# Kernel tuning notes

Hardware: AMD Instinct MI355X
Metric: run time of the kernel (lower is better)

## Reference

```python
import jax, jax.numpy as jnp
import numpy as np

N, E = 100000, 1600000
IN_F, HID, OUT_F, HEADS = 256, 128, 64, 1
C = HID // HEADS  # per-head channels (=128 for heads=1)
NEG_SLOPE = 0.2   # PyG GATConv default leaky_relu slope


def setup_inputs() -> dict:
    key = jax.random.key(0)
    ks = jax.random.split(key, 16)
    w = lambda k, shape, fan: (jax.random.normal(k, shape, jnp.float32) / np.float32(np.sqrt(fan)))
    return {
        "x": jax.random.normal(ks[0], (N, IN_F), jnp.float32),
        "edge_index": jax.random.randint(ks[1], (2, E), 0, N, dtype=jnp.int32),
        "W_in": w(ks[2], (IN_F, HID), IN_F),
        "b_in": jnp.zeros((HID,), jnp.float32),
        "W1": w(ks[3], (HID, HEADS * C), HID),
        "att_src1": w(ks[4], (HEADS, C), C),
        "att_dst1": w(ks[5], (HEADS, C), C),
        "bias1": jnp.zeros((C,), jnp.float32),
        "W2": w(ks[6], (HID, HEADS * C), HID),
        "att_src2": w(ks[7], (HEADS, C), C),
        "att_dst2": w(ks[8], (HEADS, C), C),
        "bias2": jnp.zeros((C,), jnp.float32),
        "W_out": w(ks[9], (HID, OUT_F), HID),
        "b_out": jnp.zeros((OUT_F,), jnp.float32),
    }


def gat_conv(h, src, dst, W, a_src, a_dst, bias):
    """PyG GATConv, concat=False: per-head attention, segment softmax over dst, mean over heads."""
    g = (h @ W).reshape(-1, HEADS, C)                      # [N,H,C]
    alpha_src = jnp.einsum("nhc,hc->nh", g, a_src)         # [N,H]
    alpha_dst = jnp.einsum("nhc,hc->nh", g, a_dst)         # [N,H]
    e = jax.nn.leaky_relu(alpha_src[src] + alpha_dst[dst], NEG_SLOPE)  # [E,H]
    m = jax.ops.segment_max(e, dst, num_segments=N)        # [N,H], -inf for empty segments
    m = jnp.where(jnp.isfinite(m), m, 0.0)
    p = jnp.exp(e - m[dst])
    s = jax.ops.segment_sum(p, dst, num_segments=N)        # [N,H]
    alpha = p / (s[dst] + 1e-16)                           # [E,H]
    msg = g[src] * alpha[..., None]                        # [E,H,C]  (dominant traffic)
    out = jax.ops.segment_sum(msg, dst, num_segments=N)    # [N,H,C]
    return out.mean(axis=1) + bias                         # concat=False -> head average


def reference(x, edge_index, W_in, b_in, W1, att_src1, att_dst1, bias1,
              W2, att_src2, att_dst2, bias2, W_out, b_out):
    src, dst = edge_index[0], edge_index[1]
    h = x @ W_in + b_in
    h = jax.nn.relu(gat_conv(h, src, dst, W1, att_src1, att_dst1, bias1))
    h = jax.nn.relu(gat_conv(h, src, dst, W2, att_src2, att_dst2, bias2))
    return h @ W_out + b_out
```

## Files before the change

### kernel.cpp

```cpp
#include <hip/hip_runtime.h>
#include <hip/hip_fp16.h>
#include <math.h>

#define NN 100000
#define EE 1600000
constexpr int IN_F = 256, HID = 128, OUT_F = 64;

#define NB 196
#define CAP 16384
#define CH 16384
#define NCHUNK 98

typedef __bf16 bf16x8 __attribute__((ext_vector_type(8)));
typedef float  f32x4  __attribute__((ext_vector_type(4)));

__device__ __forceinline__ f32x4 mfma16(bf16x8 a, bf16x8 b, f32x4 c){
  return __builtin_amdgcn_mfma_f32_16x16x32_bf16(a, b, c, 0, 0, 0);
}

__device__ __forceinline__ float wred_max(float v){
#pragma unroll
  for (int m=1; m<64; m<<=1) v = fmaxf(v, __shfl_xor(v, m, 64));
  return v;
}
__device__ __forceinline__ float wred_sum(float v){
#pragma unroll
  for (int m=1; m<64; m<<=1) v += __shfl_xor(v, m, 64);
  return v;
}

__global__ __launch_bounds__(256) void k_bin(const int* __restrict__ src,
    const int* __restrict__ dst, int* __restrict__ bucketCnt, int* __restrict__ recs)
{
  __shared__ int sd[CH];
  __shared__ int cnt[NB];
  __shared__ int base[NB];
  const int tid = threadIdx.x;
  const int e0 = blockIdx.x * CH;
  const int ne = min(CH, EE - e0);

  for (int i=tid; i<NB; i+=256) cnt[i] = 0;
  __syncthreads();
  for (int i=tid; i<ne; i+=256){
    int d = dst[e0+i];
    sd[i] = d;
    atomicAdd(&cnt[d>>9], 1);
  }
  __syncthreads();
  for (int i=tid; i<NB; i+=256) base[i] = atomicAdd(&bucketCnt[i], cnt[i]);
  __syncthreads();
  for (int i=tid; i<NB; i+=256) cnt[i] = 0;
  __syncthreads();
  for (int i=tid; i<ne; i+=256){
    int d = sd[i], b = d >> 9;
    int r = atomicAdd(&cnt[b], 1);
    int pos = base[b] + r;
    if (pos < CAP) recs[(size_t)b*CAP + pos] = src[e0+i] | ((d & 511) << 17);
  }
}

__global__ void k_bscan(const int* __restrict__ bucketCnt, int* __restrict__ bucketStart){
  __shared__ int sd[256];
  int t = threadIdx.x;
  int v = (t < NB) ? min(bucketCnt[t], CAP) : 0;
  sd[t] = v; __syncthreads();
#pragma unroll
  for (int off=1; off<256; off<<=1){
    int x = (t >= off) ? sd[t-off] : 0;
    __syncthreads();
    sd[t] += x;
    __syncthreads();
  }
  if (t < NB) bucketStart[t] = sd[t] - v;
}

__global__ __launch_bounds__(256) void k_csr(const int* __restrict__ recs,
    const int* __restrict__ bucketCnt, const int* __restrict__ bucketStart,
    int* __restrict__ rp, int* __restrict__ colsrc)
{
  __shared__ int hist[513];
  __shared__ int srcbuf[CAP];
  const int tid = threadIdx.x;
  const int b = blockIdx.x;
  const int cntb = min(bucketCnt[b], CAP);
  const int bstart = bucketStart[b];
  const int n0 = b << 9;
  const int nnode = min(512, NN - n0);
  const int* rb = recs + (size_t)b*CAP;

  for (int i=tid; i<513; i+=256) hist[i] = 0;
  __syncthreads();
  for (int i=tid; i<cntb; i+=256) atomicAdd(&hist[(rb[i] >> 17) + 1], 1);
  __syncthreads();
#pragma unroll
  for (int off=1; off<513; off<<=1){
    int vals[3];
    int q = 0;
    for (int i=tid; i<513; i+=256, q++) vals[q] = (i >= off) ? hist[i-off] : 0;
    __syncthreads();
    q = 0;
    for (int i=tid; i<513; i+=256, q++) hist[i] += vals[q];
    __syncthreads();
  }
  for (int l=tid; l<nnode; l+=256) rp[n0+l] = bstart + hist[l];
  if (b == 0 && tid == 0) rp[NN] = EE;
  __syncthreads();
  for (int i=tid; i<cntb; i+=256){
    int rec = rb[i];
    int r = atomicAdd(&hist[rec >> 17], 1);
    srcbuf[r] = rec & 0x1FFFF;
  }
  __syncthreads();
  for (int i=tid; i<cntb; i+=256) colsrc[bstart + i] = srcbuf[i];
}

__global__ void k_wsplit(const float* __restrict__ W, __bf16* __restrict__ hi, __bf16* __restrict__ lo,
                         int K, int N){
  int idx = blockIdx.x*256 + threadIdx.x;
  if (idx >= K*N) return;
  int k = idx / N, n = idx - k*N;
  float v = W[idx];
  __bf16 h = (__bf16)v;
  hi[(size_t)n*K + k] = h;
  lo[(size_t)n*K + k] = (__bf16)(v - (float)h);
}

template<int K, int BN, bool ATT, bool BIAS, typename OT>
__global__ __launch_bounds__(256) void k_gemm_mfma(
    const float* __restrict__ A, const __bf16* __restrict__ Bhi, const __bf16* __restrict__ Blo,
    const float* __restrict__ bias, OT* __restrict__ C,
    const float* __restrict__ attS, const float* __restrict__ attD,
    float* __restrict__ asrc, float* __restrict__ adst, int nrows)
{
  constexpr int NF = BN/16;
  __shared__ float  As[64][36];
  __shared__ __bf16 Bh[BN][56];
  __shared__ __bf16 Bl[BN][56];
  const int tid  = threadIdx.x;
  const int w    = tid >> 6, lane = tid & 63;
  const int lr   = lane & 15, lk = (lane >> 4) * 8;
  const int rowBase = blockIdx.x * 64;

  f32x4 acc[NF];
#pragma unroll
  for (int i=0;i<NF;i++) acc[i] = (f32x4)(0.f);

  const int ar = tid >> 2, aq = tid & 3;
  int agr = rowBase + ar; if (agr >= nrows) agr = nrows - 1;
  const float* aptr = A + (size_t)agr*K + aq*8;
  const int bn = tid >> 1, bhalf = tid & 1;
  const bool bact = (tid < BN*2);

  for (int kc=0; kc<K; kc+=32){
    float4 av0 = *(const float4*)(aptr + kc);
    float4 av1 = *(const float4*)(aptr + kc + 4);
    bf16x8 bh0, bh1, bl0, bl1;
    if (bact){
      const __bf16* ph = Bhi + (size_t)bn*K + kc + bhalf*16;
      const __bf16* pl = Blo + (size_t)bn*K + kc + bhalf*16;
      bh0 = *(const bf16x8*)(ph);
      bh1 = *(const bf16x8*)(ph + 8);
      bl0 = *(const bf16x8*)(pl);
      bl1 = *(const bf16x8*)(pl + 8);
    }
    __syncthreads();
    *(float4*)&As[ar][aq*8]     = av0;
    *(float4*)&As[ar][aq*8 + 4] = av1;
    if (bact){
      *(bf16x8*)&Bh[bn][bhalf*16]     = bh0;
      *(bf16x8*)&Bh[bn][bhalf*16 + 8] = bh1;
      *(bf16x8*)&Bl[bn][bhalf*16]     = bl0;
      *(bf16x8*)&Bl[bn][bhalf*16 + 8] = bl1;
    }
    __syncthreads();

    const float* arow = &As[w*16 + lr][lk];
    float4 af0 = *(const float4*)(arow);
    float4 af1 = *(const float4*)(arow + 4);
    float a8[8] = {af0.x, af0.y, af0.z, af0.w, af1.x, af1.y, af1.z, af1.w};
    bf16x8 ahi, alo;
#pragma unroll
    for (int j=0;j<8;j++){
      __bf16 h = (__bf16)a8[j];
      ahi[j] = h;
      alo[j] = (__bf16)(a8[j] - (float)h);
    }
#pragma unroll
    for (int nf=0; nf<NF; nf++){
      bf16x8 bh = *(const bf16x8*)&Bh[nf*16 + lr][lk];
      bf16x8 bl = *(const bf16x8*)&Bl[nf*16 + lr][lk];
      acc[nf] = mfma16(ahi, bh, acc[nf]);
      acc[nf] = mfma16(alo, bh, acc[nf]);
      acc[nf] = mfma16(ahi, bl, acc[nf]);
    }
  }

  const int rbase = rowBase + w*16 + (lane>>4)*4;
  if (ATT){
    float ps[4] = {0.f,0.f,0.f,0.f}, pd[4] = {0.f,0.f,0.f,0.f};
#pragma unroll
    for (int nf=0; nf<NF; nf++){
      float sv = attS[nf*16 + lr], dv = attD[nf*16 + lr];
#pragma unroll
      for (int i=0;i<4;i++){
        ps[i] = fmaf(acc[nf][i], sv, ps[i]);
        pd[i] = fmaf(acc[nf][i], dv, pd[i]);
      }
    }
#pragma unroll
    for (int m=1;m<16;m<<=1){
#pragma unroll
      for (int i=0;i<4;i++){
        ps[i] += __shfl_xor(ps[i], m, 64);
        pd[i] += __shfl_xor(pd[i], m, 64);
      }
    }
    if (lr == 0){
#pragma unroll
      for (int i=0;i<4;i++){
        int row = rbase + i;
        if (row < nrows){ asrc[row] = ps[i]; adst[row] = pd[i]; }
      }
    }
  }
#pragma unroll
  for (int i=0;i<4;i++){
    int row = rbase + i;
    if (row < nrows){
#pragma unroll
      for (int nf=0; nf<NF; nf++){
        float v = acc[nf][i] + (BIAS ? bias[nf*16 + lr] : 0.f);
        if constexpr (__is_same(OT, __half))
          C[(size_t)row*BN + nf*16 + lr] = __float2half(v);
        else
          C[(size_t)row*BN + nf*16 + lr] = v;
      }
    }
  }
}

__global__ __launch_bounds__(256) void k_agg(const __half* __restrict__ g,
    const float* __restrict__ asrc, const float* __restrict__ adst,
    const int* __restrict__ rp, const int* __restrict__ cs,
    const float* __restrict__ bias, float* __restrict__ out)
{
  int w = threadIdx.x >> 6, lane = threadIdx.x & 63;
  int node = blockIdx.x*4 + w;
  if (node >= NN) return;
  int r0 = rp[node], r1 = rp[node+1];
  int deg = r1 - r0;
  float ad = adst[node];

  float m = -INFINITY, ssum = 0.f, a0 = 0.f, a1 = 0.f;
  for (int base=0; base<deg; base+=64){
    int i = base + lane;
    bool val = i < deg;
    int sj = val ? cs[r0+i] : 0;
    float e = -INFINITY;
    if (val){ float t = asrc[sj] + ad; e = (t > 0.f) ? t : 0.2f*t; }
    float mn = fmaxf(m, wred_max(e));
    float sc = __expf(m - mn);
    float p = val ? __expf(e - mn) : 0.f;
    float psum = wred_sum(p);
    ssum = ssum*sc + psum;
    a0 *= sc; a1 *= sc;
    int cnt = min(deg - base, 64);
    int j = 0;
    for (; j + 4 <= cnt; j += 4){
      float al[4]; int ss[4];
#pragma unroll
      for (int u=0;u<4;u++){
        al[u] = __shfl(p,  j+u, 64);
        ss[u] = __shfl(sj, j+u, 64);
      }
      float2 gv[4];
#pragma unroll
      for (int u=0;u<4;u++){
        __half2 hv = *(const __half2*)(g + (size_t)ss[u]*HID + 2*lane);
        gv[u] = __half22float2(hv);
      }
#pragma unroll
      for (int u=0;u<4;u++){
        a0 = fmaf(al[u], gv[u].x, a0);
        a1 = fmaf(al[u], gv[u].y, a1);
      }
    }
    for (; j < cnt; j++){
      float alpha = __shfl(p, j, 64);
      int s = __shfl(sj, j, 64);
      __half2 hv = *(const __half2*)(g + (size_t)s*HID + 2*lane);
      float2 gvv = __half22float2(hv);
      a0 = fmaf(alpha, gvv.x, a0);
      a1 = fmaf(alpha, gvv.y, a1);
    }
    m = mn;
  }
  float inv = 1.f/(ssum + 1e-16f);
  float o0 = fmaxf(a0*inv + bias[2*lane+0], 0.f);
  float o1 = fmaxf(a1*inv + bias[2*lane+1], 0.f);
  *(float2*)(out + (size_t)node*HID + 2*lane) = make_float2(o0, o1);
}

extern "C" void kernel_launch(void* const* d_in, const int* in_sizes, int n_in,
                              void* d_out, int out_size, void* d_ws, size_t ws_size,
                              hipStream_t stream) {
  const float* x     = (const float*)d_in[0];
  const int*   ei    = (const int*)  d_in[1];
  const float* W_in  = (const float*)d_in[2];
  const float* b_in  = (const float*)d_in[3];
  const float* W1    = (const float*)d_in[4];
  const float* as1   = (const float*)d_in[5];
  const float* ad1   = (const float*)d_in[6];
  const float* bias1 = (const float*)d_in[7];
  const float* W2    = (const float*)d_in[8];
  const float* as2   = (const float*)d_in[9];
  const float* ad2   = (const float*)d_in[10];
  const float* bias2 = (const float*)d_in[11];
  const float* W_out = (const float*)d_in[12];
  const float* b_out = (const float*)d_in[13];
  float* out = (float*)d_out;

  char* ws = (char*)d_ws;
  size_t off = 0;
  auto alloc = [&](size_t bytes)->void*{ void* p = ws + off; off += (bytes + 255) & ~255ull; return p; };
  float*  bufH  = (float*) alloc((size_t)NN*HID*4);
  __half* bufG  = (__half*)alloc((size_t)NN*HID*2);
  float*  bufO  = (float*) alloc((size_t)NN*HID*4);
  float*  asrc  = (float*) alloc((size_t)NN*4);
  float*  adst  = (float*) alloc((size_t)NN*4);
  int*    rp    = (int*)   alloc((size_t)(NN+1)*4);
  int*    colsrc= (int*)   alloc((size_t)EE*4);
  int*    recs  = (int*)   alloc((size_t)NB*CAP*4);
  int*    bucketCnt   = (int*)alloc(NB*4);
  int*    bucketStart = (int*)alloc(NB*4);
  __bf16* whiI = (__bf16*)alloc((size_t)HID*IN_F*2);
  __bf16* wloI = (__bf16*)alloc((size_t)HID*IN_F*2);
  __bf16* whi1 = (__bf16*)alloc((size_t)HID*HID*2);
  __bf16* wlo1 = (__bf16*)alloc((size_t)HID*HID*2);
  __bf16* whi2 = (__bf16*)alloc((size_t)HID*HID*2);
  __bf16* wlo2 = (__bf16*)alloc((size_t)HID*HID*2);
  __bf16* whiO = (__bf16*)alloc((size_t)OUT_F*HID*2);
  __bf16* wloO = (__bf16*)alloc((size_t)OUT_F*HID*2);
  (void)ws_size; (void)in_sizes; (void)n_in; (void)out_size;

  const int* srcIdx = ei;
  const int* dstIdx = ei + EE;

  k_wsplit<<<(IN_F*HID+255)/256, 256, 0, stream>>>(W_in,  whiI, wloI, IN_F, HID);
  k_wsplit<<<(HID*HID+255)/256, 256, 0, stream>>>(W1,    whi1, wlo1, HID, HID);
  k_wsplit<<<(HID*HID+255)/256, 256, 0, stream>>>(W2,    whi2, wlo2, HID, HID);
  k_wsplit<<<(HID*OUT_F+255)/256, 256, 0, stream>>>(W_out, whiO, wloO, HID, OUT_F);

  hipMemsetAsync(bucketCnt, 0, NB*4, stream);
  k_bin  <<<NCHUNK, 256, 0, stream>>>(srcIdx, dstIdx, bucketCnt, recs);
  k_bscan<<<1, 256, 0, stream>>>(bucketCnt, bucketStart);
  k_csr  <<<NB, 256, 0, stream>>>(recs, bucketCnt, bucketStart, rp, colsrc);

  const int gblocks = (NN + 63) / 64;
  k_gemm_mfma<256,128,false,true,float><<<gblocks, 256, 0, stream>>>(x, whiI, wloI, b_in, bufH,
      nullptr, nullptr, nullptr, nullptr, NN);
  k_gemm_mfma<128,128,true,false,__half><<<gblocks, 256, 0, stream>>>(bufH, whi1, wlo1, nullptr, bufG,
      as1, ad1, asrc, adst, NN);
  k_agg<<<NN/4, 256, 0, stream>>>(bufG, asrc, adst, rp, colsrc, bias1, bufO);
  k_gemm_mfma<128,128,true,false,__half><<<gblocks, 256, 0, stream>>>(bufO, whi2, wlo2, nullptr, bufG,
      as2, ad2, asrc, adst, NN);
  k_agg<<<NN/4, 256, 0, stream>>>(bufG, asrc, adst, rp, colsrc, bias2, bufH);
  k_gemm_mfma<128,64,false,true,float><<<gblocks, 256, 0, stream>>>(bufH, whiO, wloO, b_out, out,
      nullptr, nullptr, nullptr, nullptr, NN);
}
```

Baseline: 356.2 us.

## Store activations as pre-split bf16 pairs, 128-row GEMM tiles, 16-byte gathers in aggregation

GEMM tiles grow from 64 to 128 rows per block, each wave computing two 16-row fragments so every B fragment is reused twice. Intermediate activations are stored as pre-split bf16 hi/lo pairs, so the next GEMM loads bf16 directly instead of fp32 and skips the in-kernel split. The aggregation kernel now has four edges processed in parallel per wave, with each lane loading 16 bytes and a one-step software prefetch, followed by a cross-group shuffle reduction. The aim is to cut memory traffic and instruction overhead in both the GEMMs and the gathers, at the cost of more registers and extra LDS for the A tile.

```diff
diff --git a/kernel.cpp b/kernel.cpp
--- a/kernel.cpp
+++ b/kernel.cpp
@@ -125,115 +125,145 @@
   lo[(size_t)n*K + k] = (__bf16)(v - (float)h);
 }
 
-template<int K, int BN, bool ATT, bool BIAS, typename OT>
+template<int K, int BN, bool ATT, bool BIAS, bool ASPLIT, int OMODE>
 __global__ __launch_bounds__(256) void k_gemm_mfma(
-    const float* __restrict__ A, const __bf16* __restrict__ Bhi, const __bf16* __restrict__ Blo,
-    const float* __restrict__ bias, OT* __restrict__ C,
+    const float* __restrict__ Af, const __bf16* __restrict__ AhiG, const __bf16* __restrict__ AloG,
+    const __bf16* __restrict__ Bhi, const __bf16* __restrict__ Blo,
+    const float* __restrict__ bias,
+    void* __restrict__ C0, void* __restrict__ C1,
     const float* __restrict__ attS, const float* __restrict__ attD,
     float* __restrict__ asrc, float* __restrict__ adst, int nrows)
 {
   constexpr int NF = BN/16;
-  __shared__ float  As[64][36];
+  __shared__ __bf16 Ah[128][40];
+  __shared__ __bf16 Al[128][40];
   __shared__ __bf16 Bh[BN][56];
   __shared__ __bf16 Bl[BN][56];
-  const int tid  = threadIdx.x;
-  const int w    = tid >> 6, lane = tid & 63;
-  const int lr   = lane & 15, lk = (lane >> 4) * 8;
-  const int rowBase = blockIdx.x * 64;
-
-  f32x4 acc[NF];
-#pragma unroll
-  for (int i=0;i<NF;i++) acc[i] = (f32x4)(0.f);
-
-  const int ar = tid >> 2, aq = tid & 3;
+  const int tid = threadIdx.x;
+  const int w = tid >> 6, lane = tid & 63;
+  const int lr = lane & 15, lk = (lane >> 4) * 8;
+  const int rowBase = blockIdx.x * 128;
+
+  f32x4 acc[2][NF];
+#pragma unroll
+  for (int f=0; f<2; f++)
+#pragma unroll
+    for (int nf=0; nf<NF; nf++) acc[f][nf] = (f32x4)(0.f);
+
+  const int ar = tid >> 1, ah2 = (tid & 1) * 16;
   int agr = rowBase + ar; if (agr >= nrows) agr = nrows - 1;
-  const float* aptr = A + (size_t)agr*K + aq*8;
-  const int bn = tid >> 1, bhalf = tid & 1;
-  const bool bact = (tid < BN*2);
+  const int bn = tid >> 1, bh2 = (tid & 1) * 16;
+  const bool bact = tid < BN*2;
 
   for (int kc=0; kc<K; kc+=32){
-    float4 av0 = *(const float4*)(aptr + kc);
-    float4 av1 = *(const float4*)(aptr + kc + 4);
-    bf16x8 bh0, bh1, bl0, bl1;
+    bf16x8 wh0, wh1, wl0, wl1;
+    if constexpr (ASPLIT){
+      const __bf16* ph = AhiG + (size_t)agr*K + kc + ah2;
+      const __bf16* pl = AloG + (size_t)agr*K + kc + ah2;
+      wh0 = *(const bf16x8*)ph;     wh1 = *(const bf16x8*)(ph + 8);
+      wl0 = *(const bf16x8*)pl;     wl1 = *(const bf16x8*)(pl + 8);
+    } else {
+      const float* pa = Af + (size_t)agr*K + kc + ah2;
+      float4 f0 = *(const float4*)pa,       f1 = *(const float4*)(pa + 4);
+      float4 f2 = *(const float4*)(pa + 8), f3 = *(const float4*)(pa + 12);
+      float fv[16] = {f0.x,f0.y,f0.z,f0.w, f1.x,f1.y,f1.z,f1.w,
+                      f2.x,f2.y,f2.z,f2.w, f3.x,f3.y,f3.z,f3.w};
+#pragma unroll
+      for (int u=0; u<8; u++){
+        __bf16 h = (__bf16)fv[u];
+        wh0[u] = h; wl0[u] = (__bf16)(fv[u] - (float)h);
+      }
+#pragma unroll
+      for (int u=0; u<8; u++){
+        __bf16 h = (__bf16)fv[8+u];
+        wh1[u] = h; wl1[u] = (__bf16)(fv[8+u] - (float)h);
+      }
+    }
+    bf16x8 vb0, vb1, vc0, vc1;
     if (bact){
-      const __bf16* ph = Bhi + (size_t)bn*K + kc + bhalf*16;
-      const __bf16* pl = Blo + (size_t)bn*K + kc + bhalf*16;
-      bh0 = *(const bf16x8*)(ph);
-      bh1 = *(const bf16x8*)(ph + 8);
-      bl0 = *(const bf16x8*)(pl);
-      bl1 = *(const bf16x8*)(pl + 8);
-    }
-    __syncthreads();
-    *(float4*)&As[ar][aq*8]     = av0;
-    *(float4*)&As[ar][aq*8 + 4] = av1;
+      const __bf16* ph = Bhi + (size_t)bn*K + kc + bh2;
+      const __bf16* pl = Blo + (size_t)bn*K + kc + bh2;
+      vb0 = *(const bf16x8*)ph;  vb1 = *(const bf16x8*)(ph + 8);
+      vc0 = *(const bf16x8*)pl;  vc1 = *(const bf16x8*)(pl + 8);
+    }
+    __syncthreads();
+    *(bf16x8*)&Ah[ar][ah2]     = wh0;  *(bf16x8*)&Ah[ar][ah2 + 8] = wh1;
+    *(bf16x8*)&Al[ar][ah2]     = wl0;  *(bf16x8*)&Al[ar][ah2 + 8] = wl1;
     if (bact){
-      *(bf16x8*)&Bh[bn][bhalf*16]     = bh0;
-      *(bf16x8*)&Bh[bn][bhalf*16 + 8] = bh1;
-      *(bf16x8*)&Bl[bn][bhalf*16]     = bl0;
-      *(bf16x8*)&Bl[bn][bhalf*16 + 8] = bl1;
-    }
-    __syncthreads();
-
-    const float* arow = &As[w*16 + lr][lk];
-    float4 af0 = *(const float4*)(arow);
-    float4 af1 = *(const float4*)(arow + 4);
-    float a8[8] = {af0.x, af0.y, af0.z, af0.w, af1.x, af1.y, af1.z, af1.w};
-    bf16x8 ahi, alo;
-#pragma unroll
-    for (int j=0;j<8;j++){
-      __bf16 h = (__bf16)a8[j];
-      ahi[j] = h;
-      alo[j] = (__bf16)(a8[j] - (float)h);
-    }
+      *(bf16x8*)&Bh[bn][bh2]     = vb0;  *(bf16x8*)&Bh[bn][bh2 + 8] = vb1;
+      *(bf16x8*)&Bl[bn][bh2]     = vc0;  *(bf16x8*)&Bl[bn][bh2 + 8] = vc1;
+    }
+    __syncthreads();
+
+    bf16x8 fah0 = *(const bf16x8*)&Ah[w*32 + lr][lk];
+    bf16x8 fah1 = *(const bf16x8*)&Ah[w*32 + 16 + lr][lk];
+    bf16x8 fal0 = *(const bf16x8*)&Al[w*32 + lr][lk];
+    bf16x8 fal1 = *(const bf16x8*)&Al[w*32 + 16 + lr][lk];
 #pragma unroll
     for (int nf=0; nf<NF; nf++){
       bf16x8 bh = *(const bf16x8*)&Bh[nf*16 + lr][lk];
+      acc[0][nf] = mfma16(fah0, bh, acc[0][nf]);
+      acc[1][nf] = mfma16(fah1, bh, acc[1][nf]);
+      acc[0][nf] = mfma16(fal0, bh, acc[0][nf]);
+      acc[1][nf] = mfma16(fal1, bh, acc[1][nf]);
+    }
+#pragma unroll
+    for (int nf=0; nf<NF; nf++){
       bf16x8 bl = *(const bf16x8*)&Bl[nf*16 + lr][lk];
-      acc[nf] = mfma16(ahi, bh, acc[nf]);
-      acc[nf] = mfma16(alo, bh, acc[nf]);
-      acc[nf] = mfma16(ahi, bl, acc[nf]);
-    }
-  }
-
-  const int rbase = rowBase + w*16 + (lane>>4)*4;
-  if (ATT){
-    float ps[4] = {0.f,0.f,0.f,0.f}, pd[4] = {0.f,0.f,0.f,0.f};
-#pragma unroll
-    for (int nf=0; nf<NF; nf++){
-      float sv = attS[nf*16 + lr], dv = attD[nf*16 + lr];
-#pragma unroll
-      for (int i=0;i<4;i++){
-        ps[i] = fmaf(acc[nf][i], sv, ps[i]);
-        pd[i] = fmaf(acc[nf][i], dv, pd[i]);
-      }
-    }
-#pragma unroll
-    for (int m=1;m<16;m<<=1){
-#pragma unroll
-      for (int i=0;i<4;i++){
-        ps[i] += __shfl_xor(ps[i], m, 64);
-        pd[i] += __shfl_xor(pd[i], m, 64);
-      }
-    }
-    if (lr == 0){
-#pragma unroll
-      for (int i=0;i<4;i++){
-        int row = rbase + i;
-        if (row < nrows){ asrc[row] = ps[i]; adst[row] = pd[i]; }
-      }
-    }
-  }
-#pragma unroll
-  for (int i=0;i<4;i++){
-    int row = rbase + i;
-    if (row < nrows){
+      acc[0][nf] = mfma16(fah0, bl, acc[0][nf]);
+      acc[1][nf] = mfma16(fah1, bl, acc[1][nf]);
+    }
+  }
+
+  const int rq = lane >> 4;
+#pragma unroll
+  for (int f=0; f<2; f++){
+    const int rbase = rowBase + w*32 + f*16 + rq*4;
+    if (ATT){
+      float ps[4] = {0.f,0.f,0.f,0.f}, pd[4] = {0.f,0.f,0.f,0.f};
 #pragma unroll
       for (int nf=0; nf<NF; nf++){
-        float v = acc[nf][i] + (BIAS ? bias[nf*16 + lr] : 0.f);
-        if constexpr (__is_same(OT, __half))
-          C[(size_t)row*BN + nf*16 + lr] = __float2half(v);
-        else
-          C[(size_t)row*BN + nf*16 + lr] = v;
+        float sv = attS[nf*16 + lr], dv = attD[nf*16 + lr];
+#pragma unroll
+        for (int i=0;i<4;i++){
+          ps[i] = fmaf(acc[f][nf][i], sv, ps[i]);
+          pd[i] = fmaf(acc[f][nf][i], dv, pd[i]);
+        }
+      }
+#pragma unroll
+      for (int mm=1; mm<16; mm<<=1){
+#pragma unroll
+        for (int i=0;i<4;i++){
+          ps[i] += __shfl_xor(ps[i], mm, 64);
+          pd[i] += __shfl_xor(pd[i], mm, 64);
+        }
+      }
+      if (lr == 0){
+#pragma unroll
+        for (int i=0;i<4;i++){
+          int row = rbase + i;
+          if (row < nrows){ asrc[row] = ps[i]; adst[row] = pd[i]; }
+        }
+      }
+    }
+#pragma unroll
+    for (int i=0;i<4;i++){
+      int row = rbase + i;
+      if (row < nrows){
+#pragma unroll
+        for (int nf=0; nf<NF; nf++){
+          float v = acc[f][nf][i] + (BIAS ? bias[nf*16 + lr] : 0.f);
+          size_t cidx = (size_t)row*BN + nf*16 + lr;
+          if constexpr (OMODE == 0){
+            ((float*)C0)[cidx] = v;
+          } else if constexpr (OMODE == 1){
+            ((__half*)C0)[cidx] = __float2half(v);
+          } else {
+            __bf16 h = (__bf16)v;
+            ((__bf16*)C0)[cidx] = h;
+            ((__bf16*)C1)[cidx] = (__bf16)(v - (float)h);
+          }
+        }
       }
     }
   }
@@ -242,16 +272,18 @@
 __global__ __launch_bounds__(256) void k_agg(const __half* __restrict__ g,
     const float* __restrict__ asrc, const float* __restrict__ adst,
     const int* __restrict__ rp, const int* __restrict__ cs,
-    const float* __restrict__ bias, float* __restrict__ out)
+    const float* __restrict__ bias, __bf16* __restrict__ outHi, __bf16* __restrict__ outLo)
 {
   int w = threadIdx.x >> 6, lane = threadIdx.x & 63;
   int node = blockIdx.x*4 + w;
   if (node >= NN) return;
-  int r0 = rp[node], r1 = rp[node+1];
-  int deg = r1 - r0;
+  int r0 = rp[node], deg = rp[node+1] - r0;
   float ad = adst[node];
-
-  float m = -INFINITY, ssum = 0.f, a0 = 0.f, a1 = 0.f;
+  const int eg = lane >> 4, cl = lane & 15;
+
+  float m = -INFINITY, ssum = 0.f;
+  float a[8] = {0.f,0.f,0.f,0.f,0.f,0.f,0.f,0.f};
+
   for (int base=0; base<deg; base+=64){
     int i = base + lane;
     bool val = i < deg;
@@ -263,42 +295,51 @@
     float p = val ? __expf(e - mn) : 0.f;
     float psum = wred_sum(p);
     ssum = ssum*sc + psum;
-    a0 *= sc; a1 *= sc;
+#pragma unroll
+    for (int u=0;u<8;u++) a[u] *= sc;
+
     int cnt = min(deg - base, 64);
-    int j = 0;
-    for (; j + 4 <= cnt; j += 4){
-      float al[4]; int ss[4];
+    int steps = (cnt + 3) >> 2;
+    int idx = eg;
+    float al = __shfl(p,  idx, 64);
+    int   s  = __shfl(sj, idx, 64);
+    float4 raw = *(const float4*)(g + s*HID + cl*8);
+    for (int j=0; j<steps; j++){
+      float4 curv = raw; float alc = al;
+      if (j+1 < steps){
+        idx = 4*(j+1) + eg;
+        al = __shfl(p,  idx, 64);
+        s  = __shfl(sj, idx, 64);
+        raw = *(const float4*)(g + s*HID + cl*8);
+      }
+      const __half2* hp = (const __half2*)&curv;
 #pragma unroll
       for (int u=0;u<4;u++){
-        al[u] = __shfl(p,  j+u, 64);
-        ss[u] = __shfl(sj, j+u, 64);
-      }
-      float2 gv[4];
-#pragma unroll
-      for (int u=0;u<4;u++){
-        __half2 hv = *(const __half2*)(g + (size_t)ss[u]*HID + 2*lane);
-        gv[u] = __half22float2(hv);
-      }
-#pragma unroll
-      for (int u=0;u<4;u++){
-        a0 = fmaf(al[u], gv[u].x, a0);
-        a1 = fmaf(al[u], gv[u].y, a1);
-      }
-    }
-    for (; j < cnt; j++){
-      float alpha = __shfl(p, j, 64);
-      int s = __shfl(sj, j, 64);
-      __half2 hv = *(const __half2*)(g + (size_t)s*HID + 2*lane);
-      float2 gvv = __half22float2(hv);
-      a0 = fmaf(alpha, gvv.x, a0);
-      a1 = fmaf(alpha, gvv.y, a1);
+        float2 fv = __half22float2(hp[u]);
+        a[2*u]   = fmaf(alc, fv.x, a[2*u]);
+        a[2*u+1] = fmaf(alc, fv.y, a[2*u+1]);
+      }
     }
     m = mn;
   }
-  float inv = 1.f/(ssum + 1e-16f);
-  float o0 = fmaxf(a0*inv + bias[2*lane+0], 0.f);
-  float o1 = fmaxf(a1*inv + bias[2*lane+1], 0.f);
-  *(float2*)(out + (size_t)node*HID + 2*lane) = make_float2(o0, o1);
+#pragma unroll
+  for (int u=0;u<8;u++){
+    a[u] += __shfl_xor(a[u], 16, 64);
+    a[u] += __shfl_xor(a[u], 32, 64);
+  }
+  if (eg == 0){
+    float inv = 1.f/(ssum + 1e-16f);
+    bf16x8 hv, lv;
+#pragma unroll
+    for (int u=0;u<8;u++){
+      float o = fmaxf(a[u]*inv + bias[cl*8 + u], 0.f);
+      __bf16 h = (__bf16)o;
+      hv[u] = h;
+      lv[u] = (__bf16)(o - (float)h);
+    }
+    *(bf16x8*)(outHi + (size_t)node*HID + cl*8) = hv;
+    *(bf16x8*)(outLo + (size_t)node*HID + cl*8) = lv;
+  }
 }
 
 extern "C" void kernel_launch(void* const* d_in, const int* in_sizes, int n_in,
@@ -323,14 +364,16 @@
   char* ws = (char*)d_ws;
   size_t off = 0;
   auto alloc = [&](size_t bytes)->void*{ void* p = ws + off; off += (bytes + 255) & ~255ull; return p; };
-  float*  bufH  = (float*) alloc((size_t)NN*HID*4);
-  __half* bufG  = (__half*)alloc((size_t)NN*HID*2);
-  float*  bufO  = (float*) alloc((size_t)NN*HID*4);
-  float*  asrc  = (float*) alloc((size_t)NN*4);
-  float*  adst  = (float*) alloc((size_t)NN*4);
-  int*    rp    = (int*)   alloc((size_t)(NN+1)*4);
-  int*    colsrc= (int*)   alloc((size_t)EE*4);
-  int*    recs  = (int*)   alloc((size_t)NB*CAP*4);
+  __bf16* Hhi  = (__bf16*)alloc((size_t)NN*HID*2);
+  __bf16* Hlo  = (__bf16*)alloc((size_t)NN*HID*2);
+  __half* G    = (__half*)alloc((size_t)NN*HID*2);
+  __bf16* Ohi  = (__bf16*)alloc((size_t)NN*HID*2);
+  __bf16* Olo  = (__bf16*)alloc((size_t)NN*HID*2);
+  float*  asrc = (float*) alloc((size_t)NN*4);
+  float*  adst = (float*) alloc((size_t)NN*4);
+  int*    rp   = (int*)   alloc((size_t)(NN+1)*4);
+  int*    colsrc = (int*) alloc((size_t)EE*4);
+  int*    recs   = (int*) alloc((size_t)NB*CAP*4);
   int*    bucketCnt   = (int*)alloc(NB*4);
   int*    bucketStart = (int*)alloc(NB*4);
   __bf16* whiI = (__bf16*)alloc((size_t)HID*IN_F*2);
@@ -356,15 +399,15 @@
   k_bscan<<<1, 256, 0, stream>>>(bucketCnt, bucketStart);
   k_csr  <<<NB, 256, 0, stream>>>(recs, bucketCnt, bucketStart, rp, colsrc);
 
-  const int gblocks = (NN + 63) / 64;
-  k_gemm_mfma<256,128,false,true,float><<<gblocks, 256, 0, stream>>>(x, whiI, wloI, b_in, bufH,
-      nullptr, nullptr, nullptr, nullptr, NN);
-  k_gemm_mfma<128,128,true,false,__half><<<gblocks, 256, 0, stream>>>(bufH, whi1, wlo1, nullptr, bufG,
-      as1, ad1, asrc, adst, NN);
-  k_agg<<<NN/4, 256, 0, stream>>>(bufG, asrc, adst, rp, colsrc, bias1, bufO);
-  k_gemm_mfma<128,128,true,false,__half><<<gblocks, 256, 0, stream>>>(bufO, whi2, wlo2, nullptr, bufG,
-      as2, ad2, asrc, adst, NN);
-  k_agg<<<NN/4, 256, 0, stream>>>(bufG, asrc, adst, rp, colsrc, bias2, bufH);
-  k_gemm_mfma<128,64,false,true,float><<<gblocks, 256, 0, stream>>>(bufH, whiO, wloO, b_out, out,
-      nullptr, nullptr, nullptr, nullptr, NN);
-}
+  const int gblocks = (NN + 127) / 128;
+  k_gemm_mfma<256,128,false,true,false,2><<<gblocks, 256, 0, stream>>>(
+      x, nullptr, nullptr, whiI, wloI, b_in, Hhi, Hlo, nullptr, nullptr, nullptr, nullptr, NN);
+  k_gemm_mfma<128,128,true,false,true,1><<<gblocks, 256, 0, stream>>>(
+      nullptr, Hhi, Hlo, whi1, wlo1, nullptr, G, nullptr, as1, ad1, asrc, adst, NN);
+  k_agg<<<NN/4, 256, 0, stream>>>(G, asrc, adst, rp, colsrc, bias1, Ohi, Olo);
+  k_gemm_mfma<128,128,true,false,true,1><<<gblocks, 256, 0, stream>>>(
+      nullptr, Ohi, Olo, whi2, wlo2, nullptr, G, nullptr, as2, ad2, asrc, adst, NN);
+  k_agg<<<NN/4, 256, 0, stream>>>(G, asrc, adst, rp, colsrc, bias2, Hhi, Hlo);
+  k_gemm_mfma<128,64,false,true,true,0><<<gblocks, 256, 0, stream>>>(
+      nullptr, Hhi, Hlo, whiO, wloO, b_out, out, nullptr, nullptr, nullptr, nullptr, nullptr, NN);
+}
```

Result: slower. 364.5 us (+2.3%).
